# Optimization experiments

Hardware: AMD Instinct MI355X
Metric: run time of the kernel (lower is better)

## Reference

```python
import jax, jax.numpy as jnp
import numpy as np

N = 50000      # nodes
E = 800000     # edges (avg degree 16)
DIN = 128      # node_in_channels
DE = 16        # edge_in_channels
C1 = 64        # gat1_out_channels
H1 = 1         # num_heads
C2 = 64        # gat2_out_channels
HID = 256      # Edge_hidden_dim
NEG = 0.2      # negative_slope
DCLS = 2 * C2 + DE  # edge classifier input dim = 144


def _glorot(k, shape):
    fan = sum(shape)
    return jax.random.normal(k, shape, jnp.float32) * np.float32(np.sqrt(2.0 / fan))


def setup_inputs():
    key = jax.random.key(0)
    ks = jax.random.split(key, 30)
    inp = {
        'x': jax.random.normal(ks[0], (N, DIN), jnp.float32),
        'edge_attr': jax.random.normal(ks[1], (E, DE), jnp.float32),
        # GATv2Conv layer 1
        'W1l': _glorot(ks[2], (DIN, H1 * C1)), 'b1l': jnp.zeros((H1 * C1,), jnp.float32),
        'W1r': _glorot(ks[3], (DIN, H1 * C1)), 'b1r': jnp.zeros((H1 * C1,), jnp.float32),
        'We1': _glorot(ks[4], (DE, H1 * C1)),
        'att1': _glorot(ks[5], (H1, C1)),
        'bias1': jnp.zeros((H1 * C1,), jnp.float32),
        # GATv2Conv layer 2 (heads=1, concat=False)
        'W2l': _glorot(ks[6], (H1 * C1, C2)), 'b2l': jnp.zeros((C2,), jnp.float32),
        'W2r': _glorot(ks[7], (H1 * C1, C2)), 'b2r': jnp.zeros((C2,), jnp.float32),
        'We2': _glorot(ks[8], (DE, C2)),
        'att2': _glorot(ks[9], (1, C2)),
        'bias2': jnp.zeros((C2,), jnp.float32),
        # EdgeAttentionClassifier
        'Aw1': _glorot(ks[10], (DCLS, 64)), 'Ab1': jnp.zeros((64,), jnp.float32),
        'Aw2': _glorot(ks[11], (64, 1)), 'Ab2': jnp.zeros((1,), jnp.float32),
        'Cw1': _glorot(ks[12], (DCLS, HID)), 'Cb1': jnp.zeros((HID,), jnp.float32),
        'Cw2': _glorot(ks[13], (HID, 1)), 'Cb2': jnp.zeros((1,), jnp.float32),
        'edge_index': jax.random.randint(ks[14], (2, E), 0, N, dtype=jnp.int32),
    }
    return inp


def _gatv2_layer(x, src, dst, eattr, Wl, bl, Wr, br, We, att, bias, heads, out_ch, concat):
    n = x.shape[0]
    xl = (x @ Wl + bl).reshape(n, heads, out_ch)  # source transform
    xr = (x @ Wr + br).reshape(n, heads, out_ch)  # target transform
    e = (eattr @ We).reshape(-1, heads, out_ch)
    m = xl[src] + xr[dst] + e                      # [E, H, C]
    a = jnp.einsum('ehc,hc->eh', jax.nn.leaky_relu(m, NEG), att)
    # scatter-softmax over incoming edges of each destination node
    amax = jax.ops.segment_max(a, dst, num_segments=n)
    amax = jnp.where(jnp.isfinite(amax), amax, 0.0)
    ex = jnp.exp(a - amax[dst])
    den = jax.ops.segment_sum(ex, dst, num_segments=n)
    alpha = ex / den[dst]                          # [E, H]
    out = jax.ops.segment_sum(xl[src] * alpha[:, :, None], dst, num_segments=n)
    out = out.reshape(n, heads * out_ch) if concat else out.mean(axis=1)
    return out + bias


def reference(x, edge_attr, W1l, b1l, W1r, b1r, We1, att1, bias1,
              W2l, b2l, W2r, b2r, We2, att2, bias2,
              Aw1, Ab1, Aw2, Ab2, Cw1, Cb1, Cw2, Cb2, edge_index):
    src, dst = edge_index[0], edge_index[1]
    n = x.shape[0]
    # add self loops; self-loop edge_attr = mean of incoming edge attrs (PyG fill_value='mean')
    deg = jax.ops.segment_sum(jnp.ones(src.shape, x.dtype), dst, num_segments=n)
    loop_attr = jax.ops.segment_sum(edge_attr, dst, num_segments=n) / jnp.maximum(deg, 1.0)[:, None]
    ar = jnp.arange(n, dtype=src.dtype)
    src_sl = jnp.concatenate([src, ar])
    dst_sl = jnp.concatenate([dst, ar])
    ea_sl = jnp.concatenate([edge_attr, loop_attr], axis=0)

    h = jax.nn.elu(_gatv2_layer(x, src_sl, dst_sl, ea_sl, W1l, b1l, W1r, b1r, We1, att1, bias1, H1, C1, True))
    h2 = _gatv2_layer(h, src_sl, dst_sl, ea_sl, W2l, b2l, W2r, b2r, We2, att2, bias2, 1, C2, False)

    # edge classifier on ORIGINAL edges
    ef = jnp.concatenate([h2[src], h2[dst], edge_attr], axis=-1)  # [E, 144]
    aw = jax.nn.softmax(jax.nn.relu(ef @ Aw1 + Ab1) @ Aw2 + Ab2, axis=-1)  # [E,1] -> all ones
    wf = ef * aw
    out = (jax.nn.elu(wf @ Cw1 + Cb1) @ Cw2 + Cb2).squeeze(-1)
    return out
```

## Files before the change

### kernel.cpp

```cpp
#include <hip/hip_runtime.h>
#include <math.h>

#define NN   50000
#define NE   800000
#define ESL  (NE + NN)
#define DIN1 128
#define DE   16
#define C    64
#define HID  256
#define DCLS 144
#define KP   160
#define LDA  168
#define NEGS 0.2f
#define NPB  8
#define NBLK ((NN + 255) / 256)

typedef __attribute__((ext_vector_type(8))) short  short8;
typedef __attribute__((ext_vector_type(4))) float  f32x4;

__device__ __forceinline__ ushort f2bf(float f) {
    unsigned u = __float_as_uint(f);
    u += 0x7fffu + ((u >> 16) & 1u);
    return (ushort)(u >> 16);
}
__device__ __forceinline__ float bf2f(ushort u) {
    return __uint_as_float(((unsigned)u) << 16);
}
__device__ __forceinline__ float bflo(unsigned w) { return __uint_as_float(w << 16); }
__device__ __forceinline__ float bfhi(unsigned w) { return __uint_as_float(w & 0xffff0000u); }

__global__ void k_deg(const int* __restrict__ dst, int* __restrict__ deg) {
    int e = blockIdx.x * blockDim.x + threadIdx.x;
    if (e < NE) atomicAdd(&deg[dst[e]], 1);
}

__global__ void k_scan1(const int* __restrict__ deg, int* __restrict__ rowptr,
                        int* __restrict__ bsum) {
    __shared__ int s[256];
    int t = threadIdx.x;
    int i = blockIdx.x * 256 + t;
    int v = (i < NN) ? (deg[i] + 1) : 0;
    s[t] = v;
    __syncthreads();
    for (int off = 1; off < 256; off <<= 1) {
        int u = (t >= off) ? s[t - off] : 0;
        __syncthreads();
        s[t] += u;
        __syncthreads();
    }
    if (i < NN) rowptr[i] = s[t] - v;
    if (t == 255) bsum[blockIdx.x] = s[255];
}

__global__ void k_scan2(int* __restrict__ bsum, int* __restrict__ boff) {
    __shared__ int s[256];
    int t = threadIdx.x;
    int v = (t < NBLK) ? bsum[t] : 0;
    s[t] = v;
    __syncthreads();
    for (int off = 1; off < 256; off <<= 1) {
        int u = (t >= off) ? s[t - off] : 0;
        __syncthreads();
        s[t] += u;
        __syncthreads();
    }
    if (t < NBLK) boff[t] = s[t] - v;
}

__global__ void k_scan3(int* __restrict__ rowptr, const int* __restrict__ boff) {
    int i = blockIdx.x * 256 + threadIdx.x;
    if (i < NN) rowptr[i] += boff[blockIdx.x];
    if (i == 0) rowptr[NN] = ESL;
}

__global__ void k_scatter(const int* __restrict__ src, const int* __restrict__ dst,
                          const float* __restrict__ eattr,
                          const int* __restrict__ rowptr, int* __restrict__ cursor,
                          int* __restrict__ src_perm, ushort* __restrict__ eap) {
    int e = blockIdx.x * blockDim.x + threadIdx.x;
    if (e >= NE) return;
    int d = dst[e];
    int pos = atomicAdd(&cursor[d], 1);
    int idx = rowptr[d] + pos;
    src_perm[idx] = src[e];
    const float4* p4 = (const float4*)&eattr[(size_t)e * DE];
    float4 c0 = p4[0], c1 = p4[1], c2 = p4[2], c3 = p4[3];
    short8 r0, r1;
    r0[0]=f2bf(c0.x); r0[1]=f2bf(c0.y); r0[2]=f2bf(c0.z); r0[3]=f2bf(c0.w);
    r0[4]=f2bf(c1.x); r0[5]=f2bf(c1.y); r0[6]=f2bf(c1.z); r0[7]=f2bf(c1.w);
    r1[0]=f2bf(c2.x); r1[1]=f2bf(c2.y); r1[2]=f2bf(c2.z); r1[3]=f2bf(c2.w);
    r1[4]=f2bf(c3.x); r1[5]=f2bf(c3.y); r1[6]=f2bf(c3.z); r1[7]=f2bf(c3.w);
    short8* q = (short8*)&eap[(size_t)idx * DE];
    q[0] = r0; q[1] = r1;
}

__global__ void k_loop_csr(const int* __restrict__ rowptr,
                           ushort* __restrict__ eap, int* __restrict__ src_perm) {
    int wave = threadIdx.x >> 6, lane = threadIdx.x & 63;
    int d = blockIdx.x * 4 + wave;
    if (d >= NN) return;
    int j = lane & 15, g = lane >> 4;
    int kb = rowptr[d], ke1 = rowptr[d + 1] - 1;
    float sum = 0.f;
    for (int k = kb + g; k < ke1; k += 4)
        sum += bf2f(eap[(size_t)k * DE + j]);
    sum += __shfl_xor(sum, 16);
    sum += __shfl_xor(sum, 32);
    if (lane < 16)
        eap[(size_t)ke1 * DE + lane] = f2bf(sum / fmaxf((float)(ke1 - kb), 1.0f));
    if (lane == 16) src_perm[ke1] = d;
}

template<int DINT>
__global__ void k_lin(const float* __restrict__ x,
                      const float* __restrict__ Wl, const float* __restrict__ bl,
                      const float* __restrict__ Wr, const float* __restrict__ br,
                      ushort* __restrict__ xlb, float* __restrict__ xr) {
    int i0 = blockIdx.x * NPB;
    int t = threadIdx.x;
    int c = t & (C - 1);
    const float* W = (t < C) ? Wl : Wr;
    float bb = (t < C) ? bl[c] : br[c];
    float acc[NPB];
#pragma unroll
    for (int n = 0; n < NPB; ++n) acc[n] = bb;
    for (int k = 0; k < DINT; ++k) {
        float wk = W[k * C + c];
#pragma unroll
        for (int n = 0; n < NPB; ++n)
            acc[n] = fmaf(x[(i0 + n) * DINT + k], wk, acc[n]);
    }
    if (t < C) {
#pragma unroll
        for (int n = 0; n < NPB; ++n)
            xlb[(size_t)(i0 + n) * C + c] = f2bf(acc[n]);
    } else {
#pragma unroll
        for (int n = 0; n < NPB; ++n)
            xr[(size_t)(i0 + n) * C + c] = acc[n];
    }
}

template<int DO_ELU, int OUT_BF16>
__global__ __launch_bounds__(64, 4) void k_gat(
        const int* __restrict__ src_perm, const int* __restrict__ rowptr,
        const ushort* __restrict__ eap,
        const ushort* __restrict__ xlb, const float* __restrict__ xr,
        const float* __restrict__ We, const float* __restrict__ att,
        const float* __restrict__ bias, void* __restrict__ o_) {
    int d = blockIdx.x;
    int lane = threadIdx.x;
    int g = lane >> 4, l = lane & 15;
    int c0 = l * 4;
    float wreg[DE][4];
#pragma unroll
    for (int j = 0; j < DE; ++j) {
        float4 wv = *(const float4*)&We[j * C + c0];
        wreg[j][0] = wv.x; wreg[j][1] = wv.y; wreg[j][2] = wv.z; wreg[j][3] = wv.w;
    }
    float4 av4 = *(const float4*)&att[c0];
    float attv[4] = {av4.x, av4.y, av4.z, av4.w};
    float4 xr4 = *(const float4*)&xr[(size_t)d * C + c0];
    float xrv[4] = {xr4.x, xr4.y, xr4.z, xr4.w};

    float l_run = 0.f, n_run[4] = {0.f, 0.f, 0.f, 0.f};
    int kb = rowptr[d], ke = rowptr[d + 1];
    for (int k = kb; k < ke; k += 4) {
        int kk = k + g;
        bool valid = kk < ke;
        int kidx = valid ? kk : (ke - 1);
        int s = src_perm[kidx];
        uint2 xlr = *(const uint2*)&xlb[(size_t)s * C + c0];
        float xlv[4] = {bflo(xlr.x), bfhi(xlr.x), bflo(xlr.y), bfhi(xlr.y)};
        const uint4* ep = (const uint4*)&eap[(size_t)kidx * DE];
        uint4 e0 = ep[0], e1 = ep[1];
        float m[4];
#pragma unroll
        for (int i = 0; i < 4; ++i) m[i] = xlv[i] + xrv[i];
        unsigned ew[8] = {e0.x, e0.y, e0.z, e0.w, e1.x, e1.y, e1.z, e1.w};
#pragma unroll
        for (int wji = 0; wji < 8; ++wji) {
            float elo = bflo(ew[wji]), ehi = bfhi(ew[wji]);
#pragma unroll
            for (int i = 0; i < 4; ++i) {
                m[i] = fmaf(elo, wreg[2 * wji][i], m[i]);
                m[i] = fmaf(ehi, wreg[2 * wji + 1][i], m[i]);
            }
        }
        float p = 0.f;
#pragma unroll
        for (int i = 0; i < 4; ++i) {
            float t = fmaxf(m[i], NEGS * m[i]);
            p = fmaf(t, attv[i], p);
        }
        p += __shfl_xor(p, 1);
        p += __shfl_xor(p, 2);
        p += __shfl_xor(p, 4);
        p += __shfl_xor(p, 8);
        float pe = valid ? __expf(p) : 0.f;
        l_run += pe;
#pragma unroll
        for (int i = 0; i < 4; ++i) n_run[i] = fmaf(pe, xlv[i], n_run[i]);
    }
    l_run += __shfl_xor(l_run, 16);
    l_run += __shfl_xor(l_run, 32);
#pragma unroll
    for (int i = 0; i < 4; ++i) {
        n_run[i] += __shfl_xor(n_run[i], 16);
        n_run[i] += __shfl_xor(n_run[i], 32);
    }
    if (g == 0) {
        float4 bv = *(const float4*)&bias[c0];
        float bvv[4] = {bv.x, bv.y, bv.z, bv.w};
        float res[4];
#pragma unroll
        for (int i = 0; i < 4; ++i) {
            float v = n_run[i] / l_run + bvv[i];
            if (DO_ELU) v = (v > 0.f) ? v : (__expf(v) - 1.0f);
            res[i] = v;
        }
        if (OUT_BF16) {
            uint2 pk;
            pk.x = (unsigned)f2bf(res[0]) | ((unsigned)f2bf(res[1]) << 16);
            pk.y = (unsigned)f2bf(res[2]) | ((unsigned)f2bf(res[3]) << 16);
            *(uint2*)&((ushort*)o_)[(size_t)d * C + c0] = pk;
        } else {
            float4 pk = {res[0], res[1], res[2], res[3]};
            *(float4*)&((float*)o_)[(size_t)d * C + c0] = pk;
        }
    }
}

__global__ void k_cvt_w(const float* __restrict__ Cw1, short* __restrict__ Cw1T) {
    int n = blockIdx.x;
    int k = threadIdx.x;
    Cw1T[n * KP + k] = (k < DCLS) ? (short)f2bf(Cw1[k * HID + n]) : (short)0;
}

__global__ __launch_bounds__(256, 4) void k_cls_mfma(
        const int* __restrict__ src, const int* __restrict__ dst,
        const float* __restrict__ eattr, const short* __restrict__ h2b,
        const short* __restrict__ Cw1T, const float* __restrict__ Cb1,
        const float* __restrict__ Cw2, const float* __restrict__ Cb2,
        float* __restrict__ out) {
    __shared__ short sEF[64 * LDA];
    __shared__ float sOut[64];
    int t = threadIdx.x;
    int ebase = blockIdx.x * 64;
    {
        int el = t & 63, part = t >> 6;
        int e = ebase + el;
        short8* q = (short8*)&sEF[el * LDA];
        if (part == 0) {
            const short8* p = (const short8*)&h2b[(size_t)src[e] * C];
#pragma unroll
            for (int i = 0; i < 8; ++i) q[i] = p[i];
        } else if (part == 1) {
            const short8* p = (const short8*)&h2b[(size_t)dst[e] * C];
#pragma unroll
            for (int i = 0; i < 8; ++i) q[8 + i] = p[i];
        } else if (part == 2) {
            const float4* p4 = (const float4*)&eattr[(size_t)e * DE];
            float4 c0 = p4[0], c1 = p4[1], c2 = p4[2], c3 = p4[3];
            short8 r0, r1;
            r0[0]=f2bf(c0.x); r0[1]=f2bf(c0.y); r0[2]=f2bf(c0.z); r0[3]=f2bf(c0.w);
            r0[4]=f2bf(c1.x); r0[5]=f2bf(c1.y); r0[6]=f2bf(c1.z); r0[7]=f2bf(c1.w);
            r1[0]=f2bf(c2.x); r1[1]=f2bf(c2.y); r1[2]=f2bf(c2.z); r1[3]=f2bf(c2.w);
            r1[4]=f2bf(c3.x); r1[5]=f2bf(c3.y); r1[6]=f2bf(c3.z); r1[7]=f2bf(c3.w);
            q[16] = r0; q[17] = r1;
        } else {
            short8 z = {0,0,0,0,0,0,0,0};
            q[18] = z; q[19] = z;
            sOut[el] = 0.f;
        }
    }
    __syncthreads();

    int lane = t & 63, wave = t >> 6;
    int l15 = lane & 15, quad = lane >> 4;
    f32x4 acc[4][4];
#pragma unroll
    for (int mt = 0; mt < 4; ++mt)
#pragma unroll
        for (int nt = 0; nt < 4; ++nt) {
            f32x4 z = {0.f, 0.f, 0.f, 0.f};
            acc[mt][nt] = z;
        }

    const short8* Bp = (const short8*)Cw1T;
#pragma unroll
    for (int kk = 0; kk < 5; ++kk) {
        short8 a[4], b[4];
#pragma unroll
        for (int mt = 0; mt < 4; ++mt)
            a[mt] = *(const short8*)&sEF[(mt * 16 + l15) * LDA + kk * 32 + quad * 8];
#pragma unroll
        for (int nt = 0; nt < 4; ++nt)
            b[nt] = Bp[(wave * 64 + nt * 16 + l15) * 20 + kk * 4 + quad];
#pragma unroll
        for (int mt = 0; mt < 4; ++mt)
#pragma unroll
            for (int nt = 0; nt < 4; ++nt)
                acc[mt][nt] = __builtin_amdgcn_mfma_f32_16x16x32_bf16(
                    a[mt], b[nt], acc[mt][nt], 0, 0, 0);
    }

    float cb1v[4], cw2v[4];
#pragma unroll
    for (int nt = 0; nt < 4; ++nt) {
        int n = wave * 64 + nt * 16 + l15;
        cb1v[nt] = Cb1[n];
        cw2v[nt] = Cw2[n];
    }
    float cb2 = Cb2[0];
#pragma unroll
    for (int mt = 0; mt < 4; ++mt) {
        float p[4] = {0.f, 0.f, 0.f, 0.f};
#pragma unroll
        for (int nt = 0; nt < 4; ++nt)
#pragma unroll
            for (int r = 0; r < 4; ++r) {
                float h = acc[mt][nt][r] + cb1v[nt];
                h = (h > 0.f) ? h : (__expf(h) - 1.0f);
                p[r] = fmaf(h, cw2v[nt], p[r]);
            }
#pragma unroll
        for (int r = 0; r < 4; ++r) {
#pragma unroll
            for (int off = 1; off < 16; off <<= 1)
                p[r] += __shfl_xor(p[r], off);
            if (l15 == 0) atomicAdd(&sOut[mt * 16 + quad * 4 + r], p[r]);
        }
    }
    __syncthreads();
    if (t < 64) out[ebase + t] = sOut[t] + cb2;
}

extern "C" void kernel_launch(void* const* d_in, const int* in_sizes, int n_in,
                              void* d_out, int out_size, void* d_ws, size_t ws_size,
                              hipStream_t stream) {
    const float* x     = (const float*)d_in[0];
    const float* eattr = (const float*)d_in[1];
    const float* W1l   = (const float*)d_in[2];
    const float* b1l   = (const float*)d_in[3];
    const float* W1r   = (const float*)d_in[4];
    const float* b1r   = (const float*)d_in[5];
    const float* We1   = (const float*)d_in[6];
    const float* att1  = (const float*)d_in[7];
    const float* bias1 = (const float*)d_in[8];
    const float* W2l   = (const float*)d_in[9];
    const float* b2l   = (const float*)d_in[10];
    const float* W2r   = (const float*)d_in[11];
    const float* b2r   = (const float*)d_in[12];
    const float* We2   = (const float*)d_in[13];
    const float* att2  = (const float*)d_in[14];
    const float* bias2 = (const float*)d_in[15];
    const float* Cw1   = (const float*)d_in[20];
    const float* Cb1   = (const float*)d_in[21];
    const float* Cw2   = (const float*)d_in[22];
    const float* Cb2   = (const float*)d_in[23];
    const int*   eidx  = (const int*)d_in[24];
    const int* src = eidx;
    const int* dst = eidx + NE;
    float* out = (float*)d_out;

    int*    deg      = (int*)d_ws;
    int*    cursor   = deg + NN;
    int*    rowptr   = cursor + NN;
    int*    bsum     = rowptr + NN + 4;
    int*    boff     = bsum + 256;
    int*    src_perm = boff + 256;
    ushort* eap      = (ushort*)(src_perm + ESL);
    ushort* xlb      = eap + (size_t)ESL * DE;
    float*  xr       = (float*)(xlb + (size_t)NN * C);
    float*  o1       = xr + (size_t)64 * NN;
    short*  h2b      = (short*)(o1 + (size_t)64 * NN);
    short*  cw1t     = h2b + (size_t)NN * C;

    hipMemsetAsync(deg, 0, (size_t)(2 * NN) * sizeof(int), stream);

    k_deg<<<(NE + 255) / 256, 256, 0, stream>>>(dst, deg);
    k_scan1<<<NBLK, 256, 0, stream>>>(deg, rowptr, bsum);
    k_scan2<<<1, 256, 0, stream>>>(bsum, boff);
    k_scan3<<<NBLK, 256, 0, stream>>>(rowptr, boff);
    k_scatter<<<(NE + 255) / 256, 256, 0, stream>>>(src, dst, eattr, rowptr, cursor,
                                                    src_perm, eap);
    k_loop_csr<<<(NN + 3) / 4, 256, 0, stream>>>(rowptr, eap, src_perm);

    k_cvt_w<<<HID, KP, 0, stream>>>(Cw1, cw1t);

    k_lin<DIN1><<<NN / NPB, 128, 0, stream>>>(x, W1l, b1l, W1r, b1r, xlb, xr);
    k_gat<1, 0><<<NN, 64, 0, stream>>>(src_perm, rowptr, eap, xlb, xr,
                                       We1, att1, bias1, o1);

    k_lin<C><<<NN / NPB, 128, 0, stream>>>(o1, W2l, b2l, W2r, b2r, xlb, xr);
    k_gat<0, 1><<<NN, 64, 0, stream>>>(src_perm, rowptr, eap, xlb, xr,
                                       We2, att2, bias2, h2b);

    k_cls_mfma<<<NE / 64, 256, 0, stream>>>(src, dst, eattr, h2b, cw1t, Cb1, Cw2, Cb2, out);
}
```

Before: 731.8 us.

## Fuse preprocessing kernels, inline self-loop mean into GAT, enlarge classifier tiles

Merges scan2 and scan3 into one kernel. Runs the edge scatter, self-loop index write, layer-1 linear and Cw1 transpose as independent block ranges of a single launch. The self-loop edge-attribute mean is now computed inside the first GAT pass, which removes the separate loop_csr kernel. The GAT loop now prefetches the next source index, and the classifier processes 128 edges per 512-thread block. The aim is fewer launches and less extra traffic, at the cost of more registers in GAT (launch bounds lowered to 3) and more LDS per classifier block.

```diff
diff --git a/kernel.cpp b/kernel.cpp
--- a/kernel.cpp
+++ b/kernel.cpp
@@ -12,8 +12,11 @@
 #define KP   160
 #define LDA  168
 #define NEGS 0.2f
-#define NPB  8
 #define NBLK ((NN + 255) / 256)
+
+#define SCAT_B ((NE + NN + 255) / 256)
+#define LIN1_B (NN / 16)
+#define CVT_B  ((HID * KP) / 256)
 
 typedef __attribute__((ext_vector_type(8))) short  short8;
 typedef __attribute__((ext_vector_type(4))) float  f32x4;
@@ -52,7 +55,7 @@
     if (t == 255) bsum[blockIdx.x] = s[255];
 }
 
-__global__ void k_scan2(int* __restrict__ bsum, int* __restrict__ boff) {
+__global__ void k_scan23(const int* __restrict__ bsum, int* __restrict__ rowptr) {
     __shared__ int s[256];
     int t = threadIdx.x;
     int v = (t < NBLK) ? bsum[t] : 0;
@@ -64,51 +67,82 @@
         s[t] += u;
         __syncthreads();
     }
-    if (t < NBLK) boff[t] = s[t] - v;
-}
-
-__global__ void k_scan3(int* __restrict__ rowptr, const int* __restrict__ boff) {
-    int i = blockIdx.x * 256 + threadIdx.x;
-    if (i < NN) rowptr[i] += boff[blockIdx.x];
+    int add = (blockIdx.x > 0) ? s[blockIdx.x - 1] : 0;
+    int i = blockIdx.x * 256 + t;
+    if (i < NN) rowptr[i] += add;
     if (i == 0) rowptr[NN] = ESL;
 }
 
-__global__ void k_scatter(const int* __restrict__ src, const int* __restrict__ dst,
-                          const float* __restrict__ eattr,
-                          const int* __restrict__ rowptr, int* __restrict__ cursor,
-                          int* __restrict__ src_perm, ushort* __restrict__ eap) {
-    int e = blockIdx.x * blockDim.x + threadIdx.x;
-    if (e >= NE) return;
-    int d = dst[e];
-    int pos = atomicAdd(&cursor[d], 1);
-    int idx = rowptr[d] + pos;
-    src_perm[idx] = src[e];
-    const float4* p4 = (const float4*)&eattr[(size_t)e * DE];
-    float4 c0 = p4[0], c1 = p4[1], c2 = p4[2], c3 = p4[3];
-    short8 r0, r1;
-    r0[0]=f2bf(c0.x); r0[1]=f2bf(c0.y); r0[2]=f2bf(c0.z); r0[3]=f2bf(c0.w);
-    r0[4]=f2bf(c1.x); r0[5]=f2bf(c1.y); r0[6]=f2bf(c1.z); r0[7]=f2bf(c1.w);
-    r1[0]=f2bf(c2.x); r1[1]=f2bf(c2.y); r1[2]=f2bf(c2.z); r1[3]=f2bf(c2.w);
-    r1[4]=f2bf(c3.x); r1[5]=f2bf(c3.y); r1[6]=f2bf(c3.z); r1[7]=f2bf(c3.w);
-    short8* q = (short8*)&eap[(size_t)idx * DE];
-    q[0] = r0; q[1] = r1;
-}
-
-__global__ void k_loop_csr(const int* __restrict__ rowptr,
-                           ushort* __restrict__ eap, int* __restrict__ src_perm) {
-    int wave = threadIdx.x >> 6, lane = threadIdx.x & 63;
-    int d = blockIdx.x * 4 + wave;
-    if (d >= NN) return;
-    int j = lane & 15, g = lane >> 4;
-    int kb = rowptr[d], ke1 = rowptr[d + 1] - 1;
-    float sum = 0.f;
-    for (int k = kb + g; k < ke1; k += 4)
-        sum += bf2f(eap[(size_t)k * DE + j]);
-    sum += __shfl_xor(sum, 16);
-    sum += __shfl_xor(sum, 32);
-    if (lane < 16)
-        eap[(size_t)ke1 * DE + lane] = f2bf(sum / fmaxf((float)(ke1 - kb), 1.0f));
-    if (lane == 16) src_perm[ke1] = d;
+template<int DINT>
+__device__ __forceinline__ void lin_body(
+        int lb, int t, const float* __restrict__ x,
+        const float* __restrict__ Wl, const float* __restrict__ bl,
+        const float* __restrict__ Wr, const float* __restrict__ br,
+        ushort* __restrict__ xlb, float* __restrict__ xr) {
+    int i0 = lb * 16 + (t >> 7) * 8;
+    int tt = t & 127;
+    int c = tt & 63;
+    bool isl = tt < 64;
+    const float* W = isl ? Wl : Wr;
+    float bb = isl ? bl[c] : br[c];
+    float acc[8];
+#pragma unroll
+    for (int n = 0; n < 8; ++n) acc[n] = bb;
+    for (int k = 0; k < DINT; ++k) {
+        float wk = W[k * C + c];
+#pragma unroll
+        for (int n = 0; n < 8; ++n)
+            acc[n] = fmaf(x[(size_t)(i0 + n) * DINT + k], wk, acc[n]);
+    }
+    if (isl) {
+#pragma unroll
+        for (int n = 0; n < 8; ++n)
+            xlb[(size_t)(i0 + n) * C + c] = f2bf(acc[n]);
+    } else {
+#pragma unroll
+        for (int n = 0; n < 8; ++n)
+            xr[(size_t)(i0 + n) * C + c] = acc[n];
+    }
+}
+
+__global__ void k_fused(const int* __restrict__ src, const int* __restrict__ dst,
+                        const float* __restrict__ eattr,
+                        const int* __restrict__ rowptr, int* __restrict__ cursor,
+                        int* __restrict__ src_perm, ushort* __restrict__ eap,
+                        const float* __restrict__ x,
+                        const float* __restrict__ W1l, const float* __restrict__ b1l,
+                        const float* __restrict__ W1r, const float* __restrict__ b1r,
+                        ushort* __restrict__ xlb, float* __restrict__ xr,
+                        const float* __restrict__ Cw1, short* __restrict__ Cw1T) {
+    int b = blockIdx.x;
+    int t = threadIdx.x;
+    if (b < SCAT_B) {
+        int e = b * 256 + t;
+        if (e < NE) {
+            int d = dst[e];
+            int pos = atomicAdd(&cursor[d], 1);
+            int idx = rowptr[d] + pos;
+            src_perm[idx] = src[e];
+            const float4* p4 = (const float4*)&eattr[(size_t)e * DE];
+            float4 c0 = p4[0], c1 = p4[1], c2 = p4[2], c3 = p4[3];
+            short8 r0, r1;
+            r0[0]=f2bf(c0.x); r0[1]=f2bf(c0.y); r0[2]=f2bf(c0.z); r0[3]=f2bf(c0.w);
+            r0[4]=f2bf(c1.x); r0[5]=f2bf(c1.y); r0[6]=f2bf(c1.z); r0[7]=f2bf(c1.w);
+            r1[0]=f2bf(c2.x); r1[1]=f2bf(c2.y); r1[2]=f2bf(c2.z); r1[3]=f2bf(c2.w);
+            r1[4]=f2bf(c3.x); r1[5]=f2bf(c3.y); r1[6]=f2bf(c3.z); r1[7]=f2bf(c3.w);
+            short8* q = (short8*)&eap[(size_t)idx * DE];
+            q[0] = r0; q[1] = r1;
+        } else if (e < NE + NN) {
+            int n = e - NE;
+            src_perm[rowptr[n + 1] - 1] = n;
+        }
+    } else if (b < SCAT_B + LIN1_B) {
+        lin_body<DIN1>(b - SCAT_B, t, x, W1l, b1l, W1r, b1r, xlb, xr);
+    } else {
+        int idx = (b - SCAT_B - LIN1_B) * 256 + t;
+        int n = idx / KP, k = idx - n * KP;
+        Cw1T[n * KP + k] = (k < DCLS) ? (short)f2bf(Cw1[k * HID + n]) : (short)0;
+    }
 }
 
 template<int DINT>
@@ -116,35 +150,13 @@
                       const float* __restrict__ Wl, const float* __restrict__ bl,
                       const float* __restrict__ Wr, const float* __restrict__ br,
                       ushort* __restrict__ xlb, float* __restrict__ xr) {
-    int i0 = blockIdx.x * NPB;
-    int t = threadIdx.x;
-    int c = t & (C - 1);
-    const float* W = (t < C) ? Wl : Wr;
-    float bb = (t < C) ? bl[c] : br[c];
-    float acc[NPB];
-#pragma unroll
-    for (int n = 0; n < NPB; ++n) acc[n] = bb;
-    for (int k = 0; k < DINT; ++k) {
-        float wk = W[k * C + c];
-#pragma unroll
-        for (int n = 0; n < NPB; ++n)
-            acc[n] = fmaf(x[(i0 + n) * DINT + k], wk, acc[n]);
-    }
-    if (t < C) {
-#pragma unroll
-        for (int n = 0; n < NPB; ++n)
-            xlb[(size_t)(i0 + n) * C + c] = f2bf(acc[n]);
-    } else {
-#pragma unroll
-        for (int n = 0; n < NPB; ++n)
-            xr[(size_t)(i0 + n) * C + c] = acc[n];
-    }
-}
-
-template<int DO_ELU, int OUT_BF16>
-__global__ __launch_bounds__(64, 4) void k_gat(
+    lin_body<DINT>(blockIdx.x, threadIdx.x, x, Wl, bl, Wr, br, xlb, xr);
+}
+
+template<int DO_ELU, int OUT_BF16, int SELF_INLINE>
+__global__ __launch_bounds__(64, 3) void k_gat(
         const int* __restrict__ src_perm, const int* __restrict__ rowptr,
-        const ushort* __restrict__ eap,
+        ushort* __restrict__ eap,
         const ushort* __restrict__ xlb, const float* __restrict__ xr,
         const float* __restrict__ We, const float* __restrict__ att,
         const float* __restrict__ bias, void* __restrict__ o_) {
@@ -164,44 +176,112 @@
     float xrv[4] = {xr4.x, xr4.y, xr4.z, xr4.w};
 
     float l_run = 0.f, n_run[4] = {0.f, 0.f, 0.f, 0.f};
+    float easum[DE];
+    if (SELF_INLINE) {
+#pragma unroll
+        for (int j = 0; j < DE; ++j) easum[j] = 0.f;
+    }
     int kb = rowptr[d], ke = rowptr[d + 1];
-    for (int k = kb; k < ke; k += 4) {
-        int kk = k + g;
-        bool valid = kk < ke;
-        int kidx = valid ? kk : (ke - 1);
-        int s = src_perm[kidx];
-        uint2 xlr = *(const uint2*)&xlb[(size_t)s * C + c0];
+    int kend = SELF_INLINE ? (ke - 1) : ke;
+
+    if (kend > kb) {
+        int kk0 = kb + g;
+        int s_cur = src_perm[(kk0 < kend) ? kk0 : kb];
+        for (int k = kb; k < kend; k += 4) {
+            int kk = k + g;
+            bool valid = kk < kend;
+            int kidx = valid ? kk : kb;
+            int kkn = kk + 4;
+            int s_nxt = src_perm[(kkn < kend) ? kkn : kb];
+            float validf = valid ? 1.f : 0.f;
+            uint2 xlr = *(const uint2*)&xlb[(size_t)s_cur * C + c0];
+            float xlv[4] = {bflo(xlr.x), bfhi(xlr.x), bflo(xlr.y), bfhi(xlr.y)};
+            const uint4* ep = (const uint4*)&eap[(size_t)kidx * DE];
+            uint4 e0 = ep[0], e1 = ep[1];
+            float m[4];
+#pragma unroll
+            for (int i = 0; i < 4; ++i) m[i] = xlv[i] + xrv[i];
+            unsigned ew[8] = {e0.x, e0.y, e0.z, e0.w, e1.x, e1.y, e1.z, e1.w};
+#pragma unroll
+            for (int wji = 0; wji < 8; ++wji) {
+                float elo = bflo(ew[wji]), ehi = bfhi(ew[wji]);
+#pragma unroll
+                for (int i = 0; i < 4; ++i) {
+                    m[i] = fmaf(elo, wreg[2 * wji][i], m[i]);
+                    m[i] = fmaf(ehi, wreg[2 * wji + 1][i], m[i]);
+                }
+                if (SELF_INLINE) {
+                    easum[2 * wji]     = fmaf(validf, elo, easum[2 * wji]);
+                    easum[2 * wji + 1] = fmaf(validf, ehi, easum[2 * wji + 1]);
+                }
+            }
+            float p = 0.f;
+#pragma unroll
+            for (int i = 0; i < 4; ++i) {
+                float tt = fmaxf(m[i], NEGS * m[i]);
+                p = fmaf(tt, attv[i], p);
+            }
+            p += __shfl_xor(p, 1);
+            p += __shfl_xor(p, 2);
+            p += __shfl_xor(p, 4);
+            p += __shfl_xor(p, 8);
+            float pe = valid ? __expf(p) : 0.f;
+            l_run += pe;
+#pragma unroll
+            for (int i = 0; i < 4; ++i) n_run[i] = fmaf(pe, xlv[i], n_run[i]);
+            s_cur = s_nxt;
+        }
+    }
+
+    if (SELF_INLINE) {
+#pragma unroll
+        for (int j = 0; j < DE; ++j) {
+            easum[j] += __shfl_xor(easum[j], 16);
+            easum[j] += __shfl_xor(easum[j], 32);
+        }
+        float rdeg = 1.f / fmaxf((float)(kend - kb), 1.f);
+        float mean[DE];
+#pragma unroll
+        for (int j = 0; j < DE; ++j) mean[j] = easum[j] * rdeg;
+        if (lane == 0) {
+            uint4 w0, w1;
+            w0.x = (unsigned)f2bf(mean[0])  | ((unsigned)f2bf(mean[1])  << 16);
+            w0.y = (unsigned)f2bf(mean[2])  | ((unsigned)f2bf(mean[3])  << 16);
+            w0.z = (unsigned)f2bf(mean[4])  | ((unsigned)f2bf(mean[5])  << 16);
+            w0.w = (unsigned)f2bf(mean[6])  | ((unsigned)f2bf(mean[7])  << 16);
+            w1.x = (unsigned)f2bf(mean[8])  | ((unsigned)f2bf(mean[9])  << 16);
+            w1.y = (unsigned)f2bf(mean[10]) | ((unsigned)f2bf(mean[11]) << 16);
+            w1.z = (unsigned)f2bf(mean[12]) | ((unsigned)f2bf(mean[13]) << 16);
+            w1.w = (unsigned)f2bf(mean[14]) | ((unsigned)f2bf(mean[15]) << 16);
+            uint4* q = (uint4*)&eap[(size_t)kend * DE];
+            q[0] = w0; q[1] = w1;
+        }
+        uint2 xlr = *(const uint2*)&xlb[(size_t)d * C + c0];
         float xlv[4] = {bflo(xlr.x), bfhi(xlr.x), bflo(xlr.y), bfhi(xlr.y)};
-        const uint4* ep = (const uint4*)&eap[(size_t)kidx * DE];
-        uint4 e0 = ep[0], e1 = ep[1];
         float m[4];
 #pragma unroll
-        for (int i = 0; i < 4; ++i) m[i] = xlv[i] + xrv[i];
-        unsigned ew[8] = {e0.x, e0.y, e0.z, e0.w, e1.x, e1.y, e1.z, e1.w};
-#pragma unroll
-        for (int wji = 0; wji < 8; ++wji) {
-            float elo = bflo(ew[wji]), ehi = bfhi(ew[wji]);
-#pragma unroll
-            for (int i = 0; i < 4; ++i) {
-                m[i] = fmaf(elo, wreg[2 * wji][i], m[i]);
-                m[i] = fmaf(ehi, wreg[2 * wji + 1][i], m[i]);
-            }
+        for (int i = 0; i < 4; ++i) {
+            float mv = xlv[i] + xrv[i];
+#pragma unroll
+            for (int j = 0; j < DE; ++j) mv = fmaf(mean[j], wreg[j][i], mv);
+            m[i] = mv;
         }
         float p = 0.f;
 #pragma unroll
         for (int i = 0; i < 4; ++i) {
-            float t = fmaxf(m[i], NEGS * m[i]);
-            p = fmaf(t, attv[i], p);
+            float tt = fmaxf(m[i], NEGS * m[i]);
+            p = fmaf(tt, attv[i], p);
         }
         p += __shfl_xor(p, 1);
         p += __shfl_xor(p, 2);
         p += __shfl_xor(p, 4);
         p += __shfl_xor(p, 8);
-        float pe = valid ? __expf(p) : 0.f;
+        float pe = (g == 0) ? __expf(p) : 0.f;
         l_run += pe;
 #pragma unroll
         for (int i = 0; i < 4; ++i) n_run[i] = fmaf(pe, xlv[i], n_run[i]);
     }
+
     l_run += __shfl_xor(l_run, 16);
     l_run += __shfl_xor(l_run, 32);
 #pragma unroll
@@ -231,24 +311,18 @@
     }
 }
 
-__global__ void k_cvt_w(const float* __restrict__ Cw1, short* __restrict__ Cw1T) {
-    int n = blockIdx.x;
-    int k = threadIdx.x;
-    Cw1T[n * KP + k] = (k < DCLS) ? (short)f2bf(Cw1[k * HID + n]) : (short)0;
-}
-
-__global__ __launch_bounds__(256, 4) void k_cls_mfma(
+__global__ __launch_bounds__(512, 6) void k_cls_mfma(
         const int* __restrict__ src, const int* __restrict__ dst,
         const float* __restrict__ eattr, const short* __restrict__ h2b,
         const short* __restrict__ Cw1T, const float* __restrict__ Cb1,
         const float* __restrict__ Cw2, const float* __restrict__ Cb2,
         float* __restrict__ out) {
-    __shared__ short sEF[64 * LDA];
-    __shared__ float sOut[64];
+    __shared__ short sEF[128 * LDA];
+    __shared__ float sOut[128];
     int t = threadIdx.x;
-    int ebase = blockIdx.x * 64;
+    int ebase = blockIdx.x * 128;
     {
-        int el = t & 63, part = t >> 6;
+        int el = t & 127, part = t >> 7;
         int e = ebase + el;
         short8* q = (short8*)&sEF[el * LDA];
         if (part == 0) {
@@ -277,6 +351,7 @@
     __syncthreads();
 
     int lane = t & 63, wave = t >> 6;
+    int eh = wave >> 2, nh = wave & 3;
     int l15 = lane & 15, quad = lane >> 4;
     f32x4 acc[4][4];
 #pragma unroll
@@ -293,10 +368,10 @@
         short8 a[4], b[4];
 #pragma unroll
         for (int mt = 0; mt < 4; ++mt)
-            a[mt] = *(const short8*)&sEF[(mt * 16 + l15) * LDA + kk * 32 + quad * 8];
+            a[mt] = *(const short8*)&sEF[(eh * 64 + mt * 16 + l15) * LDA + kk * 32 + quad * 8];
 #pragma unroll
         for (int nt = 0; nt < 4; ++nt)
-            b[nt] = Bp[(wave * 64 + nt * 16 + l15) * 20 + kk * 4 + quad];
+            b[nt] = Bp[(nh * 64 + nt * 16 + l15) * 20 + kk * 4 + quad];
 #pragma unroll
         for (int mt = 0; mt < 4; ++mt)
 #pragma unroll
@@ -308,7 +383,7 @@
     float cb1v[4], cw2v[4];
 #pragma unroll
     for (int nt = 0; nt < 4; ++nt) {
-        int n = wave * 64 + nt * 16 + l15;
+        int n = nh * 64 + nt * 16 + l15;
         cb1v[nt] = Cb1[n];
         cw2v[nt] = Cw2[n];
     }
@@ -329,11 +404,11 @@
 #pragma unroll
             for (int off = 1; off < 16; off <<= 1)
                 p[r] += __shfl_xor(p[r], off);
-            if (l15 == 0) atomicAdd(&sOut[mt * 16 + quad * 4 + r], p[r]);
+            if (l15 == 0) atomicAdd(&sOut[eh * 64 + mt * 16 + quad * 4 + r], p[r]);
         }
     }
     __syncthreads();
-    if (t < 64) out[ebase + t] = sOut[t] + cb2;
+    if (t < 128) out[ebase + t] = sOut[t] + cb2;
 }
 
 extern "C" void kernel_launch(void* const* d_in, const int* in_sizes, int n_in,
@@ -381,21 +456,19 @@
 
     k_deg<<<(NE + 255) / 256, 256, 0, stream>>>(dst, deg);
     k_scan1<<<NBLK, 256, 0, stream>>>(deg, rowptr, bsum);
-    k_scan2<<<1, 256, 0, stream>>>(bsum, boff);
-    k_scan3<<<NBLK, 256, 0, stream>>>(rowptr, boff);
-    k_scatter<<<(NE + 255) / 256, 256, 0, stream>>>(src, dst, eattr, rowptr, cursor,
-                                                    src_perm, eap);
-    k_loop_csr<<<(NN + 3) / 4, 256, 0, stream>>>(rowptr, eap, src_perm);
-
-    k_cvt_w<<<HID, KP, 0, stream>>>(Cw1, cw1t);
-
-    k_lin<DIN1><<<NN / NPB, 128, 0, stream>>>(x, W1l, b1l, W1r, b1r, xlb, xr);
-    k_gat<1, 0><<<NN, 64, 0, stream>>>(src_perm, rowptr, eap, xlb, xr,
-                                       We1, att1, bias1, o1);
-
-    k_lin<C><<<NN / NPB, 128, 0, stream>>>(o1, W2l, b2l, W2r, b2r, xlb, xr);
-    k_gat<0, 1><<<NN, 64, 0, stream>>>(src_perm, rowptr, eap, xlb, xr,
-                                       We2, att2, bias2, h2b);
-
-    k_cls_mfma<<<NE / 64, 256, 0, stream>>>(src, dst, eattr, h2b, cw1t, Cb1, Cw2, Cb2, out);
-}
+    k_scan23<<<NBLK, 256, 0, stream>>>(bsum, rowptr);
+
+    k_fused<<<SCAT_B + LIN1_B + CVT_B, 256, 0, stream>>>(
+        src, dst, eattr, rowptr, cursor, src_perm, eap,
+        x, W1l, b1l, W1r, b1r, xlb, xr, Cw1, cw1t);
+
+    k_gat<1, 0, 1><<<NN, 64, 0, stream>>>(src_perm, rowptr, eap, xlb, xr,
+                                          We1, att1, bias1, o1);
+
+    k_lin<C><<<NN / 16, 256, 0, stream>>>(o1, W2l, b2l, W2r, b2r, xlb, xr);
+    k_gat<0, 1, 0><<<NN, 64, 0, stream>>>(src_perm, rowptr, eap, xlb, xr,
+                                          We2, att2, bias2, h2b);
+
+    k_cls_mfma<<<NE / 128, 512, 0, stream>>>(src, dst, eattr, h2b, cw1t,
+                                             Cb1, Cw2, Cb2, out);
+}
```

New measurement: 1.053 ms. 1.44x slower.
